# Kernel optimization log

Measured on AMD Instinct MI355X. Metric: run time of the kernel, lower is better.

The kernel has to match this reference:

```python
import jax, jax.numpy as jnp
import numpy as np
from jax import lax

NUM_HEADS = 4
FIN = 4096
FOUT = 4096


def setup_inputs() -> dict:
    key = jax.random.key(0)
    k1, k2, k3, k4, k5 = jax.random.split(key, 5)
    inp = jax.random.normal(k1, (2, 2048, FIN), dtype=jnp.float32)
    # xavier-uniform-like scale for the fc weight
    lim = float(np.sqrt(6.0 / (FIN + FOUT)))
    W = jax.random.uniform(k2, (FOUT, FIN), minval=-lim, maxval=lim, dtype=jnp.float32)
    # per-head 3x3 conv kernels (Conv2d(1, 1, 3, 3) per head, stacked OIHW)
    conv_w = jax.random.normal(k3, (NUM_HEADS, 1, 3, 3), dtype=jnp.float32) * (1.0 / 3.0)
    conv_b = jax.random.normal(k4, (NUM_HEADS,), dtype=jnp.float32) * 0.1
    sk_wt = jax.random.normal(k5, (NUM_HEADS, 1, 1), dtype=jnp.float32)
    return {"inp": inp, "W": W, "conv_w": conv_w, "conv_b": conv_b, "sk_wt": sk_wt}


def _transform_weight(W, conv_w, conv_b, sk_wt):
    # W: [fout, fin] -> [num_heads, fout/num_heads, fin]
    mat = W.reshape(NUM_HEADS, FOUT // NUM_HEADS, FIN)
    # per-head 3x3 conv == grouped conv with feature_group_count = num_heads
    x = mat[None]  # [1, H=num_heads, fout/h, fin]
    y = lax.conv_general_dilated(
        x, conv_w,
        window_strides=(1, 1),
        padding=((1, 1), (1, 1)),
        feature_group_count=NUM_HEADS,
        dimension_numbers=("NCHW", "OIHW", "NCHW"),
    )[0] + conv_b[:, None, None]
    # sigmoid-gated residual: out + sigmoid(sk_wt) * mat
    out = y + jax.nn.sigmoid(sk_wt) * mat
    return out.reshape(FOUT, FIN)


def reference(inp, W, conv_w, conv_b, sk_wt):
    W_i = _transform_weight(W, conv_w, conv_b, sk_wt)
    # F.linear(inp, W_i) with bias=None
    return jnp.einsum("bsf,of->bso", inp, W_i)
```

## Files before the change

### kernel.cpp

```cpp
#include <hip/hip_runtime.h>
#include <hip/hip_bf16.h>

#define FIN 4096
#define FOUT 4096
#define HEADS 4
#define ROWS_PER_HEAD (FOUT / HEADS)
#define M_DIM 4096

typedef __attribute__((ext_vector_type(8))) short bf16x8;
typedef __attribute__((ext_vector_type(4))) float floatx4;

#define CAST_BLOCKS ((M_DIM * FIN) / (256 * 8))
#define TRANS_BLOCKS ((FOUT * FIN / 8) / 256)

__global__ __launch_bounds__(256) void prep(
    const float* __restrict__ x,
    __hip_bfloat16* __restrict__ y,
    const float* __restrict__ W,
    const float* __restrict__ cw,
    const float* __restrict__ cb,
    const float* __restrict__ sk,
    __hip_bfloat16* __restrict__ Wt) {
  if (blockIdx.x < CAST_BLOCKS) {
    int idx = blockIdx.x * 256 + threadIdx.x;
    const float4* xv = (const float4*)x;
    float4 a = xv[idx * 2];
    float4 b = xv[idx * 2 + 1];
    __hip_bfloat16 t[8];
    t[0] = __float2bfloat16(a.x); t[1] = __float2bfloat16(a.y);
    t[2] = __float2bfloat16(a.z); t[3] = __float2bfloat16(a.w);
    t[4] = __float2bfloat16(b.x); t[5] = __float2bfloat16(b.y);
    t[6] = __float2bfloat16(b.z); t[7] = __float2bfloat16(b.w);
    *(bf16x8*)(&y[(size_t)idx * 8]) = *(bf16x8*)t;
    return;
  }

  int gid = (blockIdx.x - CAST_BLOCKS) * 256 + threadIdx.x;
  int o = gid >> 9;
  int fs = (gid & 511) << 3;
  int h = o >> 10;
  int r = o & (ROWS_PER_HEAD - 1);

  float kk[3][3];
#pragma unroll
  for (int i = 0; i < 3; i++)
#pragma unroll
    for (int j = 0; j < 3; j++) kk[i][j] = cw[h * 9 + i * 3 + j];
  float sig = 1.0f / (1.0f + __expf(-sk[h]));

  float acc[8];
#pragma unroll
  for (int j = 0; j < 8; j++) acc[j] = cb[h];

#pragma unroll
  for (int dr = -1; dr <= 1; dr++) {
    int rr = r + dr;
    if (rr < 0 || rr >= ROWS_PER_HEAD) continue;
    const float* rp = W + ((size_t)(h * ROWS_PER_HEAD + rr)) * FIN + fs;
    float a[10];
    float4 v0 = *(const float4*)rp;
    float4 v1 = *(const float4*)(rp + 4);
    a[1] = v0.x; a[2] = v0.y; a[3] = v0.z; a[4] = v0.w;
    a[5] = v1.x; a[6] = v1.y; a[7] = v1.z; a[8] = v1.w;
    a[0] = (fs > 0) ? rp[-1] : 0.0f;
    a[9] = (fs + 8 < FIN) ? rp[8] : 0.0f;
#pragma unroll
    for (int j = 0; j < 8; j++)
      acc[j] += kk[dr + 1][0] * a[j] + kk[dr + 1][1] * a[j + 1] +
                kk[dr + 1][2] * a[j + 2];
    if (dr == 0) {
#pragma unroll
      for (int j = 0; j < 8; j++) acc[j] += sig * a[j + 1];
    }
  }
  __hip_bfloat16 t[8];
#pragma unroll
  for (int j = 0; j < 8; j++) t[j] = __float2bfloat16(acc[j]);
  *(bf16x8*)(&Wt[(size_t)o * FIN + fs]) = *(bf16x8*)t;
}

__device__ static inline void gload_lds16(const void* g, void* l) {
  __builtin_amdgcn_global_load_lds(
      (const __attribute__((address_space(1))) void*)g,
      (__attribute__((address_space(3))) void*)l, 16, 0, 0);
}

#define BK 64
#define NT (FIN / BK)

__global__ __launch_bounds__(512, 2) void gemm_nt(
    const __hip_bfloat16* __restrict__ A,
    const __hip_bfloat16* __restrict__ B,
    float* __restrict__ C,
    int M, int N, int K) {
  __shared__ __hip_bfloat16 As0h0[128 * BK];
  __shared__ __hip_bfloat16 As0h1[128 * BK];
  __shared__ __hip_bfloat16 As1h0[128 * BK];
  __shared__ __hip_bfloat16 As1h1[128 * BK];
  __shared__ __hip_bfloat16 Bs0h0[128 * BK];
  __shared__ __hip_bfloat16 Bs0h1[128 * BK];
  __shared__ __hip_bfloat16 Bs1h0[128 * BK];
  __shared__ __hip_bfloat16 Bs1h1[128 * BK];

  const int tid = threadIdx.x;
  const int lane = tid & 63;
  const int wave = tid >> 6;
  const int wr = wave >> 2;
  const int wn = wave & 3;
  const int fr = lane & 15;
  const int quad = lane >> 4;
  const int sel = fr & 7;

  const int orig = blockIdx.y * gridDim.x + blockIdx.x;
  const int swz = (orig & 7) * 32 + (orig >> 3);
  const int tile_m = (swz >> 4) * 256;
  const int tile_n = (swz & 15) * 256;

  const __hip_bfloat16* At = A + (size_t)tile_m * K;
  const __hip_bfloat16* Bt = B + (size_t)tile_n * K;

  int soff[2], doff[2];
#pragma unroll
  for (int c = 0; c < 2; c++) {
    int p = c * 512 + tid;
    int row = p >> 3;
    int g = (p & 7) ^ (row & 7);
    soff[c] = row * K + g * 8;
    doff[c] = p * 8;
  }
  int aro[4], bro[2], co[2];
#pragma unroll
  for (int u = 0; u < 4; u++) aro[u] = (wr * 16 + u * 32 + fr) * 64;
#pragma unroll
  for (int j = 0; j < 2; j++) bro[j] = (wn * 16 + j * 64 + fr) * 64;
#pragma unroll
  for (int kk = 0; kk < 2; kk++) co[kk] = ((kk * 4 + quad) ^ sel) * 8;

  floatx4 acc[8][4];
#pragma unroll
  for (int i = 0; i < 8; i++)
#pragma unroll
    for (int j = 0; j < 4; j++) acc[i][j] = (floatx4){0.f, 0.f, 0.f, 0.f};

  bf16x8 af[4][2];
  bf16x8 bf[2][2][2];

#define STAGE(GBASE, DST, TILE, HALF)                                    \
  do {                                                                   \
    const __hip_bfloat16* _s =                                           \
        GBASE + (size_t)(HALF) * 128 * K + (size_t)(TILE) * BK;          \
    _Pragma("unroll") for (int _c = 0; _c < 2; _c++) {                   \
      gload_lds16(_s + soff[_c], DST + doff[_c]);                        \
    }                                                                    \
  } while (0)

#define LOADA(SRC)                                                       \
  do {                                                                   \
    _Pragma("unroll") for (int _u = 0; _u < 4; _u++) {                   \
      _Pragma("unroll") for (int _kk = 0; _kk < 2; _kk++) {              \
        af[_u][_kk] = *(const bf16x8*)&SRC[aro[_u] + co[_kk]];           \
      }                                                                  \
    }                                                                    \
  } while (0)

#define LOADB(SRC, NH)                                                   \
  do {                                                                   \
    _Pragma("unroll") for (int _j = 0; _j < 2; _j++) {                   \
      _Pragma("unroll") for (int _kk = 0; _kk < 2; _kk++) {              \
        bf[NH][_j][_kk] = *(const bf16x8*)&SRC[bro[_j] + co[_kk]];       \
      }                                                                  \
    }                                                                    \
  } while (0)

#define MMA(MH, NH)                                                      \
  do {                                                                   \
    __builtin_amdgcn_s_setprio(1);                                       \
    _Pragma("unroll") for (int _kk = 0; _kk < 2; _kk++) {                \
      _Pragma("unroll") for (int _u = 0; _u < 4; _u++) {                 \
        _Pragma("unroll") for (int _j = 0; _j < 2; _j++) {               \
          acc[(MH) * 4 + _u][(NH) * 2 + _j] =                            \
              __builtin_amdgcn_mfma_f32_16x16x32_bf16(                   \
                  af[_u][_kk], bf[NH][_j][_kk],                          \
                  acc[(MH) * 4 + _u][(NH) * 2 + _j], 0, 0, 0);           \
        }                                                                \
      }                                                                  \
    }                                                                    \
    __builtin_amdgcn_s_setprio(0);                                       \
  } while (0)

#define BAR() __builtin_amdgcn_s_barrier()
#define WAITVM(N) asm volatile("s_waitcnt vmcnt(" #N ")" ::: "memory")
#define PHASE_SYNC()                                                     \
  do {                                                                   \
    __builtin_amdgcn_sched_barrier(0);                                   \
    __builtin_amdgcn_s_barrier();                                        \
    asm volatile("s_waitcnt lgkmcnt(0)");                                \
    __builtin_amdgcn_sched_barrier(0);                                   \
  } while (0)

#define TILE_BODY(T, AB0, AB1, BB0, BB1, AN1, BN0)                       \
  do {                                                                   \
    LOADA(AB0);                                                          \
    LOADB(BB0, 0);                                                       \
    STAGE(At, AN1, (T) + 1, 1);                                          \
    PHASE_SYNC();                                                        \
    MMA(0, 0);                                                           \
    BAR();                                                               \
    LOADB(BB1, 1);                                                       \
    STAGE(Bt, BN0, (T) + 1, 0);                                          \
    PHASE_SYNC();                                                        \
    MMA(0, 1);                                                           \
    BAR();                                                               \
    LOADA(AB1);                                                          \
    STAGE(At, AB0, (T) + 2, 0);                                          \
    PHASE_SYNC();                                                        \
    MMA(1, 1);                                                           \
    BAR();                                                               \
    STAGE(Bt, BB1, (T) + 2, 1);                                          \
    PHASE_SYNC();                                                        \
    MMA(1, 0);                                                           \
    WAITVM(4);                                                           \
    BAR();                                                               \
  } while (0)

  STAGE(At, As0h0, 0, 0);
  STAGE(Bt, Bs0h1, 0, 1);
  STAGE(At, As0h1, 0, 1);
  STAGE(Bt, Bs0h0, 0, 0);
  STAGE(At, As1h0, 1, 0);
  STAGE(Bt, Bs1h1, 1, 1);
  WAITVM(4);
  BAR();

#pragma unroll 1
  for (int it = 0; it < (NT - 2) / 2; ++it) {
    const int t = it * 2;
    TILE_BODY(t, As0h0, As0h1, Bs0h0, Bs0h1, As1h1, Bs1h0);
    TILE_BODY(t + 1, As1h0, As1h1, Bs1h0, Bs1h1, As0h1, Bs0h0);
  }

  {
    LOADA(As0h0);
    LOADB(Bs0h0, 0);
    STAGE(At, As1h1, NT - 1, 1);
    PHASE_SYNC();
    MMA(0, 0);
    BAR();
    LOADB(Bs0h1, 1);
    STAGE(Bt, Bs1h0, NT - 1, 0);
    PHASE_SYNC();
    MMA(0, 1);
    BAR();
    LOADA(As0h1);
    PHASE_SYNC();
    MMA(1, 1);
    BAR();
    PHASE_SYNC();
    MMA(1, 0);
    WAITVM(0);
    BAR();
  }
  {
    LOADA(As1h0);
    LOADB(Bs1h0, 0);
    PHASE_SYNC();
    MMA(0, 0);
    BAR();
    LOADB(Bs1h1, 1);
    PHASE_SYNC();
    MMA(0, 1);
    BAR();
    LOADA(As1h1);
    PHASE_SYNC();
    MMA(1, 1);
    BAR();
    PHASE_SYNC();
    MMA(1, 0);
  }

#undef TILE_BODY
#undef PHASE_SYNC
#undef STAGE
#undef LOADA
#undef LOADB
#undef MMA
#undef BAR
#undef WAITVM

#pragma unroll
  for (int i = 0; i < 8; i++) {
    int mb = tile_m + wr * 16 + i * 32 + quad * 4;
#pragma unroll
    for (int j = 0; j < 4; j++) {
      int n = tile_n + wn * 16 + j * 64 + fr;
#pragma unroll
      for (int r = 0; r < 4; r++) {
        C[(size_t)(mb + r) * N + n] = acc[i][j][r];
      }
    }
  }
}

extern "C" void kernel_launch(void* const* d_in, const int* in_sizes, int n_in,
                              void* d_out, int out_size, void* d_ws,
                              size_t ws_size, hipStream_t stream) {
  const float* inp = (const float*)d_in[0];
  const float* W = (const float*)d_in[1];
  const float* conv_w = (const float*)d_in[2];
  const float* conv_b = (const float*)d_in[3];
  const float* sk_wt = (const float*)d_in[4];
  float* out = (float*)d_out;

  __hip_bfloat16* Wt = (__hip_bfloat16*)d_ws;
  __hip_bfloat16* Ab =
      (__hip_bfloat16*)((char*)d_ws + (size_t)(32u << 20));

  prep<<<CAST_BLOCKS + TRANS_BLOCKS, 256, 0, stream>>>(inp, Ab, W, conv_w,
                                                       conv_b, sk_wt, Wt);
  dim3 grid(FOUT / 256, M_DIM / 256);
  gemm_nt<<<grid, 512, 0, stream>>>(Ab, Wt, out, M_DIM, FOUT, FIN);
}
```

Measured before the change: 304.5 us.

## Restructure GEMM main loop into fine-grained LDS/MFMA interleaved software pipeline

Replaces the four-phase tile body, which put a block-wide barrier and a full lgkmcnt(0) wait before every MFMA group, with a schedule split by K-step. LDS fragment loads for the next sub-step are interleaved with MFMA groups, using partial lgkmcnt waits and a single barrier per tile. The last MFMA group of each tile is carried into the next tile's body. Global staging now waits on vmcnt(0) each tile with a simpler two-buffer prologue. This cuts barrier stalls and hides LDS read latency behind matrix work, at the cost of more fragment registers and a fully drained global prefetch at each tile boundary.

```diff
diff --git a/kernel.cpp b/kernel.cpp
--- a/kernel.cpp
+++ b/kernel.cpp
@@ -142,8 +142,8 @@
 #pragma unroll
     for (int j = 0; j < 4; j++) acc[i][j] = (floatx4){0.f, 0.f, 0.f, 0.f};
 
-  bf16x8 af[4][2];
-  bf16x8 bf[2][2][2];
+  bf16x8 afr[2][4];
+  bf16x8 bfr[2][2][2];
 
 #define STAGE(GBASE, DST, TILE, HALF)                                    \
   do {                                                                   \
@@ -154,35 +154,29 @@
     }                                                                    \
   } while (0)
 
-#define LOADA(SRC)                                                       \
+#define LOADA4(MS, SRC, KK)                                              \
   do {                                                                   \
     _Pragma("unroll") for (int _u = 0; _u < 4; _u++) {                   \
-      _Pragma("unroll") for (int _kk = 0; _kk < 2; _kk++) {              \
-        af[_u][_kk] = *(const bf16x8*)&SRC[aro[_u] + co[_kk]];           \
-      }                                                                  \
-    }                                                                    \
-  } while (0)
-
-#define LOADB(SRC, NH)                                                   \
+      afr[MS][_u] = *(const bf16x8*)&SRC[aro[_u] + co[KK]];              \
+    }                                                                    \
+  } while (0)
+
+#define LOADB2(KS, NH, SRC, KK)                                          \
   do {                                                                   \
     _Pragma("unroll") for (int _j = 0; _j < 2; _j++) {                   \
-      _Pragma("unroll") for (int _kk = 0; _kk < 2; _kk++) {              \
-        bf[NH][_j][_kk] = *(const bf16x8*)&SRC[bro[_j] + co[_kk]];       \
-      }                                                                  \
-    }                                                                    \
-  } while (0)
-
-#define MMA(MH, NH)                                                      \
+      bfr[KS][NH][_j] = *(const bf16x8*)&SRC[bro[_j] + co[KK]];          \
+    }                                                                    \
+  } while (0)
+
+#define MMA8(MS, KS, NH)                                                 \
   do {                                                                   \
     __builtin_amdgcn_s_setprio(1);                                       \
-    _Pragma("unroll") for (int _kk = 0; _kk < 2; _kk++) {                \
-      _Pragma("unroll") for (int _u = 0; _u < 4; _u++) {                 \
-        _Pragma("unroll") for (int _j = 0; _j < 2; _j++) {               \
-          acc[(MH) * 4 + _u][(NH) * 2 + _j] =                            \
-              __builtin_amdgcn_mfma_f32_16x16x32_bf16(                   \
-                  af[_u][_kk], bf[NH][_j][_kk],                          \
-                  acc[(MH) * 4 + _u][(NH) * 2 + _j], 0, 0, 0);           \
-        }                                                                \
+    _Pragma("unroll") for (int _u = 0; _u < 4; _u++) {                   \
+      _Pragma("unroll") for (int _j = 0; _j < 2; _j++) {                 \
+        acc[(MS) * 4 + _u][(NH) * 2 + _j] =                              \
+            __builtin_amdgcn_mfma_f32_16x16x32_bf16(                     \
+                afr[MS][_u], bfr[KS][NH][_j],                            \
+                acc[(MS) * 4 + _u][(NH) * 2 + _j], 0, 0, 0);             \
       }                                                                  \
     }                                                                    \
     __builtin_amdgcn_s_setprio(0);                                       \
@@ -190,100 +184,71 @@
 
 #define BAR() __builtin_amdgcn_s_barrier()
 #define WAITVM(N) asm volatile("s_waitcnt vmcnt(" #N ")" ::: "memory")
-#define PHASE_SYNC()                                                     \
+#define FENCE_LGKM(N)                                                    \
   do {                                                                   \
     __builtin_amdgcn_sched_barrier(0);                                   \
-    __builtin_amdgcn_s_barrier();                                        \
-    asm volatile("s_waitcnt lgkmcnt(0)");                                \
+    asm volatile("s_waitcnt lgkmcnt(" #N ")" ::: "memory");              \
     __builtin_amdgcn_sched_barrier(0);                                   \
   } while (0)
 
-#define TILE_BODY(T, AB0, AB1, BB0, BB1, AN1, BN0)                       \
-  do {                                                                   \
-    LOADA(AB0);                                                          \
-    LOADB(BB0, 0);                                                       \
-    STAGE(At, AN1, (T) + 1, 1);                                          \
-    PHASE_SYNC();                                                        \
-    MMA(0, 0);                                                           \
-    BAR();                                                               \
-    LOADB(BB1, 1);                                                       \
-    STAGE(Bt, BN0, (T) + 1, 0);                                          \
-    PHASE_SYNC();                                                        \
-    MMA(0, 1);                                                           \
-    BAR();                                                               \
-    LOADA(AB1);                                                          \
-    STAGE(At, AB0, (T) + 2, 0);                                          \
-    PHASE_SYNC();                                                        \
-    MMA(1, 1);                                                           \
-    BAR();                                                               \
-    STAGE(Bt, BB1, (T) + 2, 1);                                          \
-    PHASE_SYNC();                                                        \
-    MMA(1, 0);                                                           \
-    WAITVM(4);                                                           \
-    BAR();                                                               \
+#define TBODY(T, CA0, CA1, CB0, CB1, NA0, NA1, NB0, NB1, DO_C8, DO_STAGE) \
+  do {                                                                    \
+    LOADA4(0, CA0, 0);                                                    \
+    LOADB2(0, 0, CB0, 0);                                                 \
+    LOADB2(0, 1, CB1, 0);                                                 \
+    if (DO_C8) MMA8(1, 1, 0);                         \
+    FENCE_LGKM(0);                                                        \
+    MMA8(0, 0, 0);                                                \
+    LOADA4(1, CA1, 0);                                           \
+    MMA8(0, 0, 1);                                                \
+    LOADB2(1, 0, CB0, 1);                                        \
+    LOADB2(1, 1, CB1, 1);                                                 \
+    if (DO_STAGE) {                                                       \
+      STAGE(At, NA0, (T) + 1, 0);                                         \
+      STAGE(At, NA1, (T) + 1, 1);                                         \
+    }                                                                     \
+    FENCE_LGKM(4);                                                        \
+    MMA8(1, 0, 1);                                                \
+    LOADA4(0, CA0, 1);                                           \
+    MMA8(1, 0, 0);                                                \
+    LOADA4(1, CA1, 1);                                           \
+    FENCE_LGKM(4);                                                        \
+    MMA8(0, 1, 0);                                                \
+    if (DO_STAGE) {                                                       \
+      STAGE(Bt, NB0, (T) + 1, 0);                                         \
+      STAGE(Bt, NB1, (T) + 1, 1);                                         \
+    }                                                                     \
+    MMA8(0, 1, 1);                                                \
+    FENCE_LGKM(0);                                                        \
+    MMA8(1, 1, 1);                                                \
+    if (DO_STAGE) WAITVM(0);                                              \
+    BAR();                                                                \
   } while (0)
 
   STAGE(At, As0h0, 0, 0);
-  STAGE(Bt, Bs0h1, 0, 1);
   STAGE(At, As0h1, 0, 1);
   STAGE(Bt, Bs0h0, 0, 0);
-  STAGE(At, As1h0, 1, 0);
-  STAGE(Bt, Bs1h1, 1, 1);
-  WAITVM(4);
+  STAGE(Bt, Bs0h1, 0, 1);
+  WAITVM(0);
   BAR();
 
+  TBODY(0, As0h0, As0h1, Bs0h0, Bs0h1, As1h0, As1h1, Bs1h0, Bs1h1, 0, 1);
+
 #pragma unroll 1
-  for (int it = 0; it < (NT - 2) / 2; ++it) {
-    const int t = it * 2;
-    TILE_BODY(t, As0h0, As0h1, Bs0h0, Bs0h1, As1h1, Bs1h0);
-    TILE_BODY(t + 1, As1h0, As1h1, Bs1h0, Bs1h1, As0h1, Bs0h0);
-  }
-
-  {
-    LOADA(As0h0);
-    LOADB(Bs0h0, 0);
-    STAGE(At, As1h1, NT - 1, 1);
-    PHASE_SYNC();
-    MMA(0, 0);
-    BAR();
-    LOADB(Bs0h1, 1);
-    STAGE(Bt, Bs1h0, NT - 1, 0);
-    PHASE_SYNC();
-    MMA(0, 1);
-    BAR();
-    LOADA(As0h1);
-    PHASE_SYNC();
-    MMA(1, 1);
-    BAR();
-    PHASE_SYNC();
-    MMA(1, 0);
-    WAITVM(0);
-    BAR();
-  }
-  {
-    LOADA(As1h0);
-    LOADB(Bs1h0, 0);
-    PHASE_SYNC();
-    MMA(0, 0);
-    BAR();
-    LOADB(Bs1h1, 1);
-    PHASE_SYNC();
-    MMA(0, 1);
-    BAR();
-    LOADA(As1h1);
-    PHASE_SYNC();
-    MMA(1, 1);
-    BAR();
-    PHASE_SYNC();
-    MMA(1, 0);
-  }
-
-#undef TILE_BODY
-#undef PHASE_SYNC
+  for (int t = 1; t < NT - 1; t += 2) {
+    TBODY(t, As1h0, As1h1, Bs1h0, Bs1h1, As0h0, As0h1, Bs0h0, Bs0h1, 1, 1);
+    TBODY(t + 1, As0h0, As0h1, Bs0h0, Bs0h1, As1h0, As1h1, Bs1h0, Bs1h1, 1, 1);
+  }
+
+  TBODY(NT - 1, As1h0, As1h1, Bs1h0, Bs1h1, As0h0, As0h1, Bs0h0, Bs0h1, 1, 0);
+  MMA8(1, 1, 0);
+
+#undef TBODY
+#undef FENCE_LGKM
 #undef STAGE
-#undef LOADA
-#undef LOADB
-#undef MMA
+#undef LOADA4
+#undef LOADB2
+#undef MMA8
 #undef BAR
 #undef WAITVM
 
```

After: 287.5 us. 5.6% less time.

## Reorder LDS staging pipeline in GEMM main loop with finer waitcnt control

Applied to the files above, without the earlier changes.

Restructures the double-buffered GEMM main loop. Global-to-LDS stage issues are now placed at different phases, the prologue preloads one more half-tile, and the explicit sched_barrier/lgkmcnt phase syncs are replaced with lighter lgkmcnt/vmcnt waits around barriers. The goal is to keep more global loads in flight and to reduce stalls between LDS reads and MFMA blocks. In exchange, the buffer-reuse ordering becomes harder to reason about and races between staging and reads are possible if a barrier is misplaced.

```diff
diff --git a/kernel.cpp b/kernel.cpp
--- a/kernel.cpp
+++ b/kernel.cpp
@@ -154,7 +154,7 @@
     }                                                                    \
   } while (0)
 
-#define LOADA(SRC)                                                       \
+#define LOADA_H(SRC)                                                     \
   do {                                                                   \
     _Pragma("unroll") for (int _u = 0; _u < 4; _u++) {                   \
       _Pragma("unroll") for (int _kk = 0; _kk < 2; _kk++) {              \
@@ -163,7 +163,7 @@
     }                                                                    \
   } while (0)
 
-#define LOADB(SRC, NH)                                                   \
+#define LOADB_H(NH, SRC)                                                 \
   do {                                                                   \
     _Pragma("unroll") for (int _j = 0; _j < 2; _j++) {                   \
       _Pragma("unroll") for (int _kk = 0; _kk < 2; _kk++) {              \
@@ -172,7 +172,7 @@
     }                                                                    \
   } while (0)
 
-#define MMA(MH, NH)                                                      \
+#define MMA16(MH, NH)                                                    \
   do {                                                                   \
     __builtin_amdgcn_s_setprio(1);                                       \
     _Pragma("unroll") for (int _kk = 0; _kk < 2; _kk++) {                \
@@ -189,103 +189,78 @@
   } while (0)
 
 #define BAR() __builtin_amdgcn_s_barrier()
-#define WAITVM(N) asm volatile("s_waitcnt vmcnt(" #N ")" ::: "memory")
-#define PHASE_SYNC()                                                     \
-  do {                                                                   \
-    __builtin_amdgcn_sched_barrier(0);                                   \
-    __builtin_amdgcn_s_barrier();                                        \
-    asm volatile("s_waitcnt lgkmcnt(0)");                                \
-    __builtin_amdgcn_sched_barrier(0);                                   \
-  } while (0)
-
-#define TILE_BODY(T, AB0, AB1, BB0, BB1, AN1, BN0)                       \
-  do {                                                                   \
-    LOADA(AB0);                                                          \
-    LOADB(BB0, 0);                                                       \
-    STAGE(At, AN1, (T) + 1, 1);                                          \
-    PHASE_SYNC();                                                        \
-    MMA(0, 0);                                                           \
-    BAR();                                                               \
-    LOADB(BB1, 1);                                                       \
-    STAGE(Bt, BN0, (T) + 1, 0);                                          \
-    PHASE_SYNC();                                                        \
-    MMA(0, 1);                                                           \
-    BAR();                                                               \
-    LOADA(AB1);                                                          \
-    STAGE(At, AB0, (T) + 2, 0);                                          \
-    PHASE_SYNC();                                                        \
-    MMA(1, 1);                                                           \
-    BAR();                                                               \
-    STAGE(Bt, BB1, (T) + 2, 1);                                          \
-    PHASE_SYNC();                                                        \
-    MMA(1, 0);                                                           \
-    WAITVM(4);                                                           \
-    BAR();                                                               \
-  } while (0)
+#define VMC(N) asm volatile("s_waitcnt vmcnt(" #N ")" ::: "memory")
+#define LGKM(N) asm volatile("s_waitcnt lgkmcnt(" #N ")" ::: "memory")
 
   STAGE(At, As0h0, 0, 0);
+  STAGE(Bt, Bs0h0, 0, 0);
   STAGE(Bt, Bs0h1, 0, 1);
   STAGE(At, As0h1, 0, 1);
-  STAGE(Bt, Bs0h0, 0, 0);
   STAGE(At, As1h0, 1, 0);
   STAGE(Bt, Bs1h1, 1, 1);
-  WAITVM(4);
+  STAGE(At, As1h1, 1, 1);
+  VMC(6);
   BAR();
 
 #pragma unroll 1
-  for (int it = 0; it < (NT - 2) / 2; ++it) {
-    const int t = it * 2;
-    TILE_BODY(t, As0h0, As0h1, Bs0h0, Bs0h1, As1h1, Bs1h0);
-    TILE_BODY(t + 1, As1h0, As1h1, Bs1h0, Bs1h1, As0h1, Bs0h0);
+  for (int it = 0; it < (NT / 2) - 1; ++it) {
+    const int T = it * 2;
+    LOADA_H(As0h0);
+    LOADB_H(0, Bs0h0);
+    STAGE(Bt, Bs1h0, T + 1, 0);
+    LGKM(8);
+    BAR(); LGKM(0); MMA16(0, 0); BAR();
+    LOADB_H(1, Bs0h1);
+    STAGE(At, As0h0, T + 2, 0);
+    BAR(); LGKM(0); MMA16(0, 1); BAR();
+    LOADA_H(As0h1);
+    STAGE(Bt, Bs0h1, T + 2, 1);
+    BAR(); LGKM(0); MMA16(1, 1); BAR();
+    STAGE(At, As0h1, T + 2, 1);
+    BAR(); MMA16(1, 0); VMC(6); BAR();
+    LOADA_H(As1h0);
+    LOADB_H(0, Bs1h0);
+    STAGE(Bt, Bs0h0, T + 2, 0);
+    LGKM(8);
+    BAR(); LGKM(0); MMA16(0, 0); BAR();
+    LOADB_H(1, Bs1h1);
+    STAGE(At, As1h0, T + 3, 0);
+    BAR(); LGKM(0); MMA16(0, 1); BAR();
+    LOADA_H(As1h1);
+    STAGE(Bt, Bs1h1, T + 3, 1);
+    BAR(); LGKM(0); MMA16(1, 1); BAR();
+    STAGE(At, As1h1, T + 3, 1);
+    BAR(); MMA16(1, 0); VMC(6); BAR();
   }
 
   {
-    LOADA(As0h0);
-    LOADB(Bs0h0, 0);
-    STAGE(At, As1h1, NT - 1, 1);
-    PHASE_SYNC();
-    MMA(0, 0);
-    BAR();
-    LOADB(Bs0h1, 1);
+    LOADA_H(As0h0);
+    LOADB_H(0, Bs0h0);
     STAGE(Bt, Bs1h0, NT - 1, 0);
-    PHASE_SYNC();
-    MMA(0, 1);
-    BAR();
-    LOADA(As0h1);
-    PHASE_SYNC();
-    MMA(1, 1);
-    BAR();
-    PHASE_SYNC();
-    MMA(1, 0);
-    WAITVM(0);
-    BAR();
-  }
-  {
-    LOADA(As1h0);
-    LOADB(Bs1h0, 0);
-    PHASE_SYNC();
-    MMA(0, 0);
-    BAR();
-    LOADB(Bs1h1, 1);
-    PHASE_SYNC();
-    MMA(0, 1);
-    BAR();
-    LOADA(As1h1);
-    PHASE_SYNC();
-    MMA(1, 1);
-    BAR();
-    PHASE_SYNC();
-    MMA(1, 0);
-  }
-
-#undef TILE_BODY
-#undef PHASE_SYNC
+    LGKM(8);
+    BAR(); LGKM(0); MMA16(0, 0); BAR();
+    LOADB_H(1, Bs0h1);
+    BAR(); LGKM(0); MMA16(0, 1); BAR();
+    LOADA_H(As0h1);
+    BAR(); LGKM(0); MMA16(1, 1); BAR();
+    BAR(); MMA16(1, 0); VMC(0); BAR();
+    LOADA_H(As1h0);
+    LOADB_H(0, Bs1h0);
+    BAR(); LGKM(0); MMA16(0, 0); BAR();
+    LOADB_H(1, Bs1h1);
+    BAR(); LGKM(0); MMA16(0, 1); BAR();
+    LOADA_H(As1h1);
+    BAR(); LGKM(0); MMA16(1, 1); BAR();
+    BAR(); MMA16(1, 0);
+  }
+
 #undef STAGE
-#undef LOADA
-#undef LOADB
-#undef MMA
+#undef LOADA_H
+#undef LOADB_H
+#undef MMA16
 #undef BAR
-#undef WAITVM
+#undef VMC
+#undef LGKM
 
 #pragma unroll
   for (int i = 0; i < 8; i++) {
```

After: 293.7 us. -3.5%, faster.
